# Kernel optimization log

Hardware: AMD Instinct MI355X
Metric: run time of the kernel (lower is better)

## Reference

```python
import jax, jax.numpy as jnp
import numpy as np

D = 512      # embed_dim
H = 8        # num_heads
DEPTH = 3    # decoder layers
V = 10000    # vocab_size
B = 64       # batch
NIMG = 144   # image grid tokens
SEQ = 17     # caption length (get_clip_mat(17,144))
FF = 4 * D


def layer_norm(x, g, b, eps=1e-5):
    m = jnp.mean(x, axis=-1, keepdims=True)
    v = jnp.mean((x - m) ** 2, axis=-1, keepdims=True)
    return (x - m) * jax.lax.rsqrt(v + eps) * g + b


def mha(xq, xkv, wq, bq, wk, bk, wv, bv, wo, bo):
    # torch MultiHeadSelfAttention with mask=None
    Bq, Nq, Dm = xq.shape
    hd = Dm // H
    q = (xq @ wq + bq).reshape(Bq, Nq, H, hd)
    k = (xkv @ wk + bk).reshape(Bq, -1, H, hd)
    v = (xkv @ wv + bv).reshape(Bq, -1, H, hd)
    attn = jnp.einsum('bqhd,bkhd->bhqk', q, k) * (hd ** -0.5)
    attn = jax.nn.softmax(attn, axis=-1)
    out = jnp.einsum('bhqk,bkhd->bqhd', attn, v).reshape(Bq, Nq, Dm)
    return out @ wo + bo


def setup_inputs() -> dict:
    key = jax.random.key(0)
    ks = iter(jax.random.split(key, 64))
    def p(*shape):
        return jax.random.normal(next(ks), shape, dtype=jnp.float32) * 0.02
    inp = {
        'encoder_out': jax.random.normal(next(ks), (B, NIMG, D), dtype=jnp.float32),
        'w': jax.random.uniform(next(ks), (SEQ, NIMG), dtype=jnp.float32) / NIMG,
        # img2text: Linear + LayerNorm
        'i2t_w': p(D, D), 'i2t_b': jnp.zeros((D,), jnp.float32),
        'i2t_ln_g': jnp.ones((D,), jnp.float32), 'i2t_ln_b': jnp.zeros((D,), jnp.float32),
        'emb': p(V, D),                                   # word_embed table
        'gen_w': p(D, V), 'gen_b': jnp.zeros((V,), jnp.float32),  # generator
        'a_w': p(2 * D, D), 'a_b': jnp.zeros((D,), jnp.float32),  # a_embed gate
        'fln_g': jnp.ones((D,), jnp.float32), 'fln_b': jnp.zeros((D,), jnp.float32),
        # stacked per-layer params [DEPTH, ...]
        'sa_wq': p(DEPTH, D, D), 'sa_bq': jnp.zeros((DEPTH, D), jnp.float32),
        'sa_wk': p(DEPTH, D, D), 'sa_bk': jnp.zeros((DEPTH, D), jnp.float32),
        'sa_wv': p(DEPTH, D, D), 'sa_bv': jnp.zeros((DEPTH, D), jnp.float32),
        'sa_wo': p(DEPTH, D, D), 'sa_bo': jnp.zeros((DEPTH, D), jnp.float32),
        'ca_wq': p(DEPTH, D, D), 'ca_bq': jnp.zeros((DEPTH, D), jnp.float32),
        'ca_wk': p(DEPTH, D, D), 'ca_bk': jnp.zeros((DEPTH, D), jnp.float32),
        'ca_wv': p(DEPTH, D, D), 'ca_bv': jnp.zeros((DEPTH, D), jnp.float32),
        'ca_wo': p(DEPTH, D, D), 'ca_bo': jnp.zeros((DEPTH, D), jnp.float32),
        'ln1_g': jnp.ones((DEPTH, D), jnp.float32), 'ln1_b': jnp.zeros((DEPTH, D), jnp.float32),
        'ln2_g': jnp.ones((DEPTH, D), jnp.float32), 'ln2_b': jnp.zeros((DEPTH, D), jnp.float32),
        'ln3_g': jnp.ones((DEPTH, D), jnp.float32), 'ln3_b': jnp.zeros((DEPTH, D), jnp.float32),
        'fc1_w': p(DEPTH, D, FF), 'fc1_b': jnp.zeros((DEPTH, FF), jnp.float32),
        'fc2_w': p(DEPTH, FF, D), 'fc2_b': jnp.zeros((DEPTH, D), jnp.float32),
    }
    return inp


def reference(encoder_out, w, i2t_w, i2t_b, i2t_ln_g, i2t_ln_b, emb, gen_w, gen_b,
              a_w, a_b, fln_g, fln_b,
              sa_wq, sa_bq, sa_wk, sa_bk, sa_wv, sa_bv, sa_wo, sa_bo,
              ca_wq, ca_bq, ca_wk, ca_bk, ca_wv, ca_bv, ca_wo, ca_bo,
              ln1_g, ln1_b, ln2_g, ln2_b, ln3_g, ln3_b,
              fc1_w, fc1_b, fc2_w, fc2_b):
    # img2text (dropout = eval no-op)
    text_emb = layer_norm(encoder_out @ i2t_w + i2t_b, i2t_ln_g, i2t_ln_b)  # [B,NIMG,D]
    # vocab-softmax word embedding gating
    word_prob = jax.nn.softmax(jnp.einsum('bnd,vd->bnv', text_emb, emb), axis=-1)
    word_emb = text_emb + jnp.einsum('bnv,vd->bnd', word_prob, emb)
    # map 144 image tokens -> 17 caption slots
    x = jnp.einsum('sn,bnd->bsd', w, word_emb)  # [B,SEQ,D]
    x_self = x
    for i in range(DEPTH):
        sc = x
        x = mha(x, x, sa_wq[i], sa_bq[i], sa_wk[i], sa_bk[i], sa_wv[i], sa_bv[i], sa_wo[i], sa_bo[i])
        x_self = x
        x = layer_norm(x + sc, ln1_g[i], ln1_b[i])
        sc = x
        x = mha(x, encoder_out, ca_wq[i], ca_bq[i], ca_wk[i], ca_bk[i], ca_wv[i], ca_bv[i], ca_wo[i], ca_bo[i])
        x = layer_norm(x + sc, ln2_g[i], ln2_b[i])
        sc = x
        x = jax.nn.relu(x @ fc1_w[i] + fc1_b[i]) @ fc2_w[i] + fc2_b[i]
        x = layer_norm(x + sc, ln3_g[i], ln3_b[i])
    # sigmoid-gated blend of last layer output and last self-attn output
    g = jax.nn.sigmoid(jnp.concatenate([x, x_self], axis=2) @ a_w + a_b)
    x = layer_norm(x * g + x_self * (1.0 - g), fln_g, fln_b)
    out = x @ gen_w + gen_b  # [B,SEQ,V]
    return out
```

## Files before the change

### kernel.cpp

```cpp
#include <hip/hip_runtime.h>

typedef unsigned short u16;
typedef __attribute__((ext_vector_type(8))) short s16x8;
typedef __attribute__((ext_vector_type(4))) float f32x4;

__device__ __forceinline__ u16 f2bf(float x) {
    union { float f; unsigned int u; } v; v.f = x;
    return (u16)((v.u + 0x7fffu + ((v.u >> 16) & 1u)) >> 16);
}
__device__ __forceinline__ float bf2f(u16 u) {
    union { unsigned int u; float f; } v; v.u = ((unsigned int)u) << 16;
    return v.f;
}

__device__ __forceinline__ void gload_lds16(const void* g, void* l) {
    __builtin_amdgcn_global_load_lds((const __attribute__((address_space(1))) void*)g,
                                     (__attribute__((address_space(3))) void*)l, 16, 0, 0);
}

template<int BM, int BN, int WM, int WN, int MODE>
__global__ __launch_bounds__(256)
void k_gemm(const u16* __restrict__ A, int lda, const u16* __restrict__ B, int ldb,
            float* __restrict__ Cf, int ldcf, u16* __restrict__ Cb, int ldcb,
            const float* __restrict__ bias, int relu, float* __restrict__ rowsum,
            int M, int N, int Ktot, int ksplit, long czstride)
{
    constexpr int MT = WM / 16, NT = WN / 16, WC = BN / WN;
    constexpr int AI = (BM * 4) / 256, BI = (BN * 4) / 256;
    __shared__ __align__(16) u16 As[BM * 32];
    __shared__ __align__(16) u16 Bs[BN * 32];
    int tid = threadIdx.x, w = tid >> 6, lane = tid & 63;
    int m0 = blockIdx.y * BM, n0 = blockIdx.x * BN;
    int wr = w / WC, wc = w % WC, lm = lane & 15, kq = lane >> 4;
    int kbeg = blockIdx.z * ksplit;
    int kend = kbeg + ksplit; if (kend > Ktot) kend = Ktot;
    if (czstride) Cf += (size_t)blockIdx.z * czstride;

    f32x4 acc[MT][NT] = {};

    for (int k0 = kbeg; k0 < kend; k0 += 32) {
        __syncthreads();
#pragma unroll
        for (int i = 0; i < AI; ++i) {
            int c = i * 256 + tid;
            const u16* g = A + (size_t)(m0 + (c >> 2)) * lda + k0 + ((c & 3) << 3);
            gload_lds16(g, As + (size_t)(i * 256 + w * 64) * 8);
        }
#pragma unroll
        for (int i = 0; i < BI; ++i) {
            int c = i * 256 + tid;
            const u16* g = B + (size_t)(n0 + (c >> 2)) * ldb + k0 + ((c & 3) << 3);
            gload_lds16(g, Bs + (size_t)(i * 256 + w * 64) * 8);
        }
        __syncthreads();
        s16x8 af[MT], bfr[NT];
#pragma unroll
        for (int mi = 0; mi < MT; ++mi)
            af[mi] = *(const s16x8*)&As[((wr * WM + mi * 16 + lm) << 5) + (kq << 3)];
#pragma unroll
        for (int ni = 0; ni < NT; ++ni)
            bfr[ni] = *(const s16x8*)&Bs[((wc * WN + ni * 16 + lm) << 5) + (kq << 3)];
#pragma unroll
        for (int mi = 0; mi < MT; ++mi)
#pragma unroll
            for (int ni = 0; ni < NT; ++ni)
                acc[mi][ni] = __builtin_amdgcn_mfma_f32_16x16x32_bf16(af[mi], bfr[ni], acc[mi][ni], 0, 0, 0);
    }

    if constexpr (MODE == 1) {
#pragma unroll
        for (int mi = 0; mi < MT; ++mi) {
            int rb = m0 + wr * WM + mi * 16 + kq * 4;
#pragma unroll
            for (int r = 0; r < 4; ++r) {
                int row = rb + r;
                float ps = 0.f;
#pragma unroll
                for (int ni = 0; ni < NT; ++ni) {
                    int col = n0 + wc * WN + ni * 16 + lm;
                    float e = 0.f;
                    if (col < N) { e = __expf(acc[mi][ni][r]); ps += e; }
                    if (row < M) Cb[(size_t)row * ldcb + col] = f2bf(e);
                }
                ps += __shfl_xor(ps, 1); ps += __shfl_xor(ps, 2);
                ps += __shfl_xor(ps, 4); ps += __shfl_xor(ps, 8);
                if (lm == 0 && row < M) atomicAdd(rowsum + row, ps);
            }
        }
    } else {
#pragma unroll
        for (int mi = 0; mi < MT; ++mi) {
            int rb = m0 + wr * WM + mi * 16 + kq * 4;
#pragma unroll
            for (int ni = 0; ni < NT; ++ni) {
                int col = n0 + wc * WN + ni * 16 + lm;
                if (col >= N) continue;
                float bv = bias ? bias[col] : 0.f;
#pragma unroll
                for (int r = 0; r < 4; ++r) {
                    int row = rb + r;
                    if (row >= M) continue;
                    float v = acc[mi][ni][r] + bv;
                    if (relu) v = fmaxf(v, 0.f);
                    if (Cf) Cf[(size_t)row * ldcf + col] = v;
                    if (Cb) Cb[(size_t)row * ldcb + col] = f2bf(v);
                }
            }
        }
    }
}

__global__ __launch_bounds__(256)
void k_transpose(const float* __restrict__ in, long in_zs, u16* __restrict__ out, long out_zs,
                 int R, int C, int Rpad, int Cpad, int ldout)
{
    __shared__ float tile[32][33];
    const float* src = in + (size_t)blockIdx.z * in_zs;
    u16* dst = out + (size_t)blockIdx.z * out_zs;
    int c0 = blockIdx.x * 32, r0 = blockIdx.y * 32;
    int tx = threadIdx.x, ty = threadIdx.y;
#pragma unroll
    for (int i = 0; i < 32; i += 8) {
        int r = r0 + ty + i, c = c0 + tx;
        tile[ty + i][tx] = (r < R && c < C) ? src[(size_t)r * C + c] : 0.f;
    }
    __syncthreads();
#pragma unroll
    for (int i = 0; i < 32; i += 8) {
        int c = c0 + ty + i, r = r0 + tx;
        if (c < Cpad && r < Rpad) dst[(size_t)c * ldout + r] = f2bf(tile[tx][ty + i]);
    }
}

__global__ __launch_bounds__(256)
void k_cvt(const float* __restrict__ in, u16* __restrict__ out, int n)
{
    for (int i = blockIdx.x * 256 + threadIdx.x; i < n; i += gridDim.x * 256)
        out[i] = f2bf(in[i]);
}

__global__ __launch_bounds__(256)
void k_zero(float* __restrict__ p, int n)
{
    int i = blockIdx.x * 256 + threadIdx.x;
    if (i < n) p[i] = 0.f;
}

__global__ __launch_bounds__(256)
void k_biaspack(const float* __restrict__ sbq, const float* __restrict__ sbk, const float* __restrict__ sbv,
                const float* __restrict__ cbk, const float* __restrict__ cbv,
                float* __restrict__ sout, float* __restrict__ cout)
{
    int i = blockIdx.x * 256 + threadIdx.x;
    if (i < 4608) {
        int l = i / 1536, j = i % 1536;
        sout[i] = j < 512 ? sbq[l * 512 + j] : j < 1024 ? sbk[l * 512 + j - 512] : sbv[l * 512 + j - 1024];
    }
    if (i < 3072) {
        int l = i / 1024, j = i % 1024;
        cout[i] = j < 512 ? cbk[l * 512 + j] : cbv[l * 512 + j - 512];
    }
}

__global__ __launch_bounds__(256)
void k_reduce_we(const float* __restrict__ part, long ps,
                 const float* __restrict__ text, const float* __restrict__ rs,
                 float* __restrict__ out, int n)
{
    int i = blockIdx.x * 256 + threadIdx.x;
    if (i >= n) return;
    float s = 0.f;
#pragma unroll
    for (int z = 0; z < 8; ++z) s += part[(size_t)z * ps + i];
    out[i] = text[i] + s * (1.f / rs[i >> 9]);
}

__global__ __launch_bounds__(256)
void k_ln(const float* __restrict__ xin, const float* __restrict__ res,
          const float* __restrict__ g, const float* __restrict__ b,
          float* __restrict__ out, u16* __restrict__ out_bf, int ldbf)
{
    int row = blockIdx.x, t = threadIdx.x;
    size_t base = (size_t)row * 512;
    float v0 = xin[base + t], v1 = xin[base + t + 256];
    if (res) { v0 += res[base + t]; v1 += res[base + t + 256]; }
    float s1 = v0 + v1, s2 = v0 * v0 + v1 * v1;
#pragma unroll
    for (int o = 32; o > 0; o >>= 1) { s1 += __shfl_down(s1, o); s2 += __shfl_down(s2, o); }
    __shared__ float a1[4], a2[4], mr[2];
    if ((t & 63) == 0) { a1[t >> 6] = s1; a2[t >> 6] = s2; }
    __syncthreads();
    if (t == 0) {
        float S1 = a1[0] + a1[1] + a1[2] + a1[3];
        float S2 = a2[0] + a2[1] + a2[2] + a2[3];
        float m = S1 * (1.f / 512.f);
        float var = S2 * (1.f / 512.f) - m * m;
        mr[0] = m; mr[1] = rsqrtf(var + 1e-5f);
    }
    __syncthreads();
    float m = mr[0], rs = mr[1];
    float y0 = (v0 - m) * rs * g[t] + b[t];
    float y1 = (v1 - m) * rs * g[t + 256] + b[t + 256];
    out[base + t] = y0; out[base + t + 256] = y1;
    if (out_bf) {
        size_t bb = (size_t)row * ldbf;
        out_bf[bb + t] = f2bf(y0); out_bf[bb + t + 256] = f2bf(y1);
    }
}

__global__ __launch_bounds__(256)
void k_wmap(const float* __restrict__ w, const float* __restrict__ we,
            float* __restrict__ x, u16* __restrict__ x_bf)
{
    int bid = blockIdx.x;
    int b = bid / 17, s = bid % 17;
    int t = threadIdx.x;
    const float* wr = w + s * 144;
    const float* base = we + (size_t)b * 144 * 512;
    float a0 = 0.f, a1 = 0.f;
    for (int n = 0; n < 144; ++n) {
        float wv = wr[n];
        a0 += wv * base[(size_t)n * 512 + t];
        a1 += wv * base[(size_t)n * 512 + t + 256];
    }
    size_t r = (size_t)(b * 17 + s);
    x[r * 512 + t] = a0; x[r * 512 + t + 256] = a1;
    x_bf[r * 1024 + t] = f2bf(a0); x_bf[r * 1024 + t + 256] = f2bf(a1);
}

__global__ __launch_bounds__(128)
void k_attn_self(const u16* __restrict__ qkv, u16* __restrict__ o)
{
    int b = blockIdx.x >> 3, h = blockIdx.x & 7;
    __shared__ float qs[17][65], ks[17][65], vs[17][65], ps[17][18];
    int t = threadIdx.x;
    for (int i = t; i < 17 * 64; i += 128) {
        int s = i >> 6, d = i & 63;
        size_t g = ((size_t)(b * 17 + s)) * 1536 + h * 64 + d;
        qs[s][d] = bf2f(qkv[g]); ks[s][d] = bf2f(qkv[g + 512]); vs[s][d] = bf2f(qkv[g + 1024]);
    }
    __syncthreads();
    for (int i = t; i < 17 * 17; i += 128) {
        int r = i / 17, c = i % 17;
        float a = 0.f;
#pragma unroll
        for (int d = 0; d < 64; ++d) a += qs[r][d] * ks[c][d];
        ps[r][c] = a * 0.125f;
    }
    __syncthreads();
    if (t < 17) {
        float mxv = -1e30f;
        for (int c = 0; c < 17; ++c) mxv = fmaxf(mxv, ps[t][c]);
        float sm = 0.f;
        for (int c = 0; c < 17; ++c) { float e = __expf(ps[t][c] - mxv); ps[t][c] = e; sm += e; }
        float inv = 1.f / sm;
        for (int c = 0; c < 17; ++c) ps[t][c] *= inv;
    }
    __syncthreads();
    for (int i = t; i < 17 * 64; i += 128) {
        int s = i >> 6, d = i & 63;
        float a = 0.f;
#pragma unroll
        for (int j = 0; j < 17; ++j) a += ps[s][j] * vs[j][d];
        o[((size_t)(b * 17 + s)) * 512 + h * 64 + d] = f2bf(a);
    }
}

__global__ __launch_bounds__(256)
void k_attn_cross(const u16* __restrict__ q, const u16* __restrict__ kv, u16* __restrict__ o)
{
    int b = blockIdx.x >> 3, h = blockIdx.x & 7;
    __shared__ float qs[17][65];
    __shared__ float ps[17][145];
    int t = threadIdx.x;
    for (int i = t; i < 17 * 64; i += 256) {
        int s = i >> 6, d = i & 63;
        qs[s][d] = bf2f(q[((size_t)(b * 17 + s)) * 512 + h * 64 + d]);
    }
    __syncthreads();
    for (int i = t; i < 17 * 144; i += 256) {
        int r = i / 144, c = i % 144;
        const u16* kr = kv + ((size_t)(b * 144 + c)) * 3072 + h * 64;
        float a = 0.f;
#pragma unroll
        for (int d = 0; d < 64; ++d) a += qs[r][d] * bf2f(kr[d]);
        ps[r][c] = a * 0.125f;
    }
    __syncthreads();
    if (t < 17) {
        float mxv = -1e30f;
        for (int c = 0; c < 144; ++c) mxv = fmaxf(mxv, ps[t][c]);
        float sm = 0.f;
        for (int c = 0; c < 144; ++c) { float e = __expf(ps[t][c] - mxv); ps[t][c] = e; sm += e; }
        float inv = 1.f / sm;
        for (int c = 0; c < 144; ++c) ps[t][c] *= inv;
    }
    __syncthreads();
    for (int i = t; i < 17 * 64; i += 256) {
        int s = i >> 6, d = i & 63;
        float a = 0.f;
        for (int j = 0; j < 144; ++j)
            a += ps[s][j] * bf2f(kv[((size_t)(b * 144 + j)) * 3072 + 512 + h * 64 + d]);
        o[((size_t)(b * 17 + s)) * 512 + h * 64 + d] = f2bf(a);
    }
}

__global__ __launch_bounds__(256)
void k_blend(const float* __restrict__ x, const float* __restrict__ xs,
             const float* __restrict__ gl, float* __restrict__ y, int n)
{
    int i = blockIdx.x * 256 + threadIdx.x;
    if (i < n) {
        float s = 1.f / (1.f + __expf(-gl[i]));
        y[i] = x[i] * s + xs[i] * (1.f - s);
    }
}

extern "C" void kernel_launch(void* const* d_in, const int* in_sizes, int n_in,
                              void* d_out, int out_size, void* d_ws, size_t ws_size,
                              hipStream_t stream)
{
    (void)in_sizes; (void)out_size;
    if (n_in < 39) return;
    const float* enc    = (const float*)d_in[0];
    const float* wmat   = (const float*)d_in[1];
    const float* i2t_w  = (const float*)d_in[2];
    const float* i2t_b  = (const float*)d_in[3];
    const float* i2t_g  = (const float*)d_in[4];
    const float* i2t_bb = (const float*)d_in[5];
    const float* emb    = (const float*)d_in[6];
    const float* gen_w  = (const float*)d_in[7];
    const float* gen_b  = (const float*)d_in[8];
    const float* a_w    = (const float*)d_in[9];
    const float* a_b    = (const float*)d_in[10];
    const float* fln_g  = (const float*)d_in[11];
    const float* fln_b  = (const float*)d_in[12];
    const float* sa_wq  = (const float*)d_in[13];
    const float* sa_bq  = (const float*)d_in[14];
    const float* sa_wk  = (const float*)d_in[15];
    const float* sa_bk  = (const float*)d_in[16];
    const float* sa_wv  = (const float*)d_in[17];
    const float* sa_bv  = (const float*)d_in[18];
    const float* sa_wo  = (const float*)d_in[19];
    const float* sa_bo  = (const float*)d_in[20];
    const float* ca_wq  = (const float*)d_in[21];
    const float* ca_bq  = (const float*)d_in[22];
    const float* ca_wk  = (const float*)d_in[23];
    const float* ca_bk  = (const float*)d_in[24];
    const float* ca_wv  = (const float*)d_in[25];
    const float* ca_bv  = (const float*)d_in[26];
    const float* ca_wo  = (const float*)d_in[27];
    const float* ca_bo  = (const float*)d_in[28];
    const float* ln1_g  = (const float*)d_in[29];
    const float* ln1_b  = (const float*)d_in[30];
    const float* ln2_g  = (const float*)d_in[31];
    const float* ln2_b  = (const float*)d_in[32];
    const float* ln3_g  = (const float*)d_in[33];
    const float* ln3_b  = (const float*)d_in[34];
    const float* fc1_w  = (const float*)d_in[35];
    const float* fc1_b  = (const float*)d_in[36];
    const float* fc2_w  = (const float*)d_in[37];
    const float* fc2_b  = (const float*)d_in[38];

    char* ws = (char*)d_ws;
    size_t off = 0;
    auto AL = [](size_t x) { return (x + 255) & ~(size_t)255; };
    auto alloc = [&](size_t bytes) { char* p = ws + off; off += AL(bytes); return p; };

    u16* i2t_wT  = (u16*)alloc((size_t)512 * 512 * 2);
    u16* sa_qkvT = (u16*)alloc((size_t)3 * 1536 * 512 * 2);
    u16* sa_woT  = (u16*)alloc((size_t)3 * 512 * 512 * 2);
    u16* ca_qT   = (u16*)alloc((size_t)3 * 512 * 512 * 2);
    u16* ca_kvT  = (u16*)alloc((size_t)3 * 1024 * 512 * 2);
    u16* ca_woT  = (u16*)alloc((size_t)3 * 512 * 512 * 2);
    u16* fc1T    = (u16*)alloc((size_t)3 * 2048 * 512 * 2);
    u16* fc2T    = (u16*)alloc((size_t)3 * 512 * 2048 * 2);
    u16* a_wT    = (u16*)alloc((size_t)512 * 1024 * 2);
    u16* gen_wT  = (u16*)alloc((size_t)10112 * 512 * 2);
    u16* embB    = (u16*)alloc((size_t)10112 * 512 * 2);
    u16* embT    = (u16*)alloc((size_t)512 * 10112 * 2);
    u16* enc_bf  = (u16*)alloc((size_t)9216 * 512 * 2);
    float* text_f   = (float*)alloc((size_t)9216 * 512 * 4);
    u16*   text_bf  = (u16*)alloc((size_t)9216 * 512 * 2);
    float* word_emb = (float*)alloc((size_t)9216 * 512 * 4);
    float* rowsum   = (float*)alloc(9216 * 4);
    float* sa_qkvB  = (float*)alloc(4608 * 4);
    float* ca_kvB   = (float*)alloc(3072 * 4);

    u16* enc_kv = (u16*)alloc((size_t)9216 * 3072 * 2);
    u16* xcat   = (u16*)alloc((size_t)1088 * 1024 * 2);
    u16* tqkv   = (u16*)alloc((size_t)1088 * 1536 * 2);
    u16* attnb  = (u16*)alloc((size_t)1088 * 512 * 2);
    u16* q_bf   = (u16*)alloc((size_t)1088 * 512 * 2);
    u16* ffn    = (u16*)alloc((size_t)1088 * 2048 * 2);
    float* x_f   = (float*)alloc((size_t)1088 * 512 * 4);
    float* xs_f  = (float*)alloc((size_t)1088 * 512 * 4);
    float* tmp_f = (float*)alloc((size_t)1088 * 512 * 4);
    float* glin  = (float*)alloc((size_t)1088 * 512 * 4);

    size_t lo = off;
    long budget = (ws_size > lo) ? (long)(ws_size - lo) : 0;
    long perrow = 10112L * 2 + 8L * 512 * 4;
    int chunk = (int)((budget / perrow) & ~(long)127);
    if (chunk > 9216) chunk = 9216;
    if (chunk < 128) chunk = 128;
    u16* logits = (u16*)(ws + lo);
    float* part = (float*)(ws + lo + AL((size_t)chunk * 10112 * 2));
    long pstride = (long)chunk * 512;

    dim3 tb(32, 8);
    auto T = [&](const float* in, long izs, u16* out, long ozs, int R, int C, int Rp, int Cp, int ldo, int nz) {
        k_transpose<<<dim3((Cp + 31) / 32, (Rp + 31) / 32, nz), tb, 0, stream>>>(in, izs, out, ozs, R, C, Rp, Cp, ldo);
    };
    T(i2t_w, 0, i2t_wT, 0, 512, 512, 512, 512, 512, 1);
    T(sa_wq, 512 * 512, sa_qkvT,             1536 * 512, 512, 512, 512, 512, 512, 3);
    T(sa_wk, 512 * 512, sa_qkvT + 512 * 512, 1536 * 512, 512, 512, 512, 512, 512, 3);
    T(sa_wv, 512 * 512, sa_qkvT + 1024 * 512,1536 * 512, 512, 512, 512, 512, 512, 3);
    T(sa_wo, 512 * 512, sa_woT, 512 * 512, 512, 512, 512, 512, 512, 3);
    T(ca_wq, 512 * 512, ca_qT,  512 * 512, 512, 512, 512, 512, 512, 3);
    T(ca_wk, 512 * 512, ca_kvT,             1024 * 512, 512, 512, 512, 512, 512, 3);
    T(ca_wv, 512 * 512, ca_kvT + 512 * 512, 1024 * 512, 512, 512, 512, 512, 512, 3);
    T(ca_wo, 512 * 512, ca_woT, 512 * 512, 512, 512, 512, 512, 512, 3);
    T(fc1_w, (long)512 * 2048, fc1T, (long)2048 * 512, 512, 2048, 512, 2048, 512, 3);
    T(fc2_w, (long)2048 * 512, fc2T, (long)512 * 2048, 2048, 512, 2048, 512, 2048, 3);
    T(a_w, 0, a_wT, 0, 1024, 512, 1024, 512, 1024, 1);
    T(gen_w, 0, gen_wT, 0, 512, 10000, 512, 10112, 512, 1);
    T(emb, 0, embT, 0, 10000, 512, 10112, 512, 10112, 1);
    k_cvt<<<2048, 256, 0, stream>>>(emb, embB, 10000 * 512);
    k_cvt<<<2048, 256, 0, stream>>>(enc, enc_bf, 9216 * 512);
    k_biaspack<<<18, 256, 0, stream>>>(sa_bq, sa_bk, sa_bv, ca_bk, ca_bv, sa_qkvB, ca_kvB);
    k_zero<<<36, 256, 0, stream>>>(rowsum, 9216);

    k_gemm<64, 64, 32, 32, 0><<<dim3(8, 144), 256, 0, stream>>>(
        enc_bf, 512, i2t_wT, 512, word_emb, 512, nullptr, 0, i2t_b, 0, nullptr,
        9216, 512, 512, 512, 0);
    k_ln<<<9216, 256, 0, stream>>>(word_emb, nullptr, i2t_g, i2t_bb, text_f, text_bf, 512);

    for (int r0 = 0; r0 < 9216; r0 += chunk) {
        int CR = (9216 - r0 < chunk) ? (9216 - r0) : chunk;
        k_gemm<128, 128, 64, 64, 1><<<dim3(79, CR / 128), 256, 0, stream>>>(
            text_bf + (size_t)r0 * 512, 512, embB, 512, nullptr, 0, logits, 10112,
            nullptr, 0, rowsum + r0, CR, 10000, 512, 512, 0);
        k_gemm<128, 128, 64, 64, 0><<<dim3(4, CR / 128, 8), 256, 0, stream>>>(
            logits, 10112, embT, 10112, part, 512, nullptr, 0, nullptr, 0, nullptr,
            CR, 512, 10112, 1280, pstride);
        k_reduce_we<<<(CR * 512 + 255) / 256, 256, 0, stream>>>(
            part, pstride, text_f + (size_t)r0 * 512, rowsum + r0,
            word_emb + (size_t)r0 * 512, CR * 512);
    }

    k_wmap<<<1088, 256, 0, stream>>>(wmat, word_emb, x_f, xcat);

    k_gemm<128, 128, 64, 64, 0><<<dim3(24, 72), 256, 0, stream>>>(
        enc_bf, 512, ca_kvT, 512, nullptr, 0, enc_kv, 3072, ca_kvB, 0, nullptr,
        9216, 3072, 512, 512, 0);

    for (int l = 0; l < 3; ++l) {
        size_t wo = (size_t)l * 512 * 512;
        k_gemm<64, 64, 32, 32, 0><<<dim3(24, 17), 256, 0, stream>>>(
            xcat, 1024, sa_qkvT + (size_t)l * 1536 * 512, 512, nullptr, 0, tqkv, 1536,
            sa_qkvB + l * 1536, 0, nullptr, 1088, 1536, 512, 512, 0);
        k_attn_self<<<512, 128, 0, stream>>>(tqkv, attnb);
        k_gemm<64, 64, 32, 32, 0><<<dim3(8, 17), 256, 0, stream>>>(
            attnb, 512, sa_woT + wo, 512, xs_f, 512, xcat + 512, 1024,
            sa_bo + l * 512, 0, nullptr, 1088, 512, 512, 512, 0);
        k_ln<<<1088, 256, 0, stream>>>(xs_f, x_f, ln1_g + l * 512, ln1_b + l * 512, x_f, xcat, 1024);
        k_gemm<64, 64, 32, 32, 0><<<dim3(8, 17), 256, 0, stream>>>(
            xcat, 1024, ca_qT + wo, 512, nullptr, 0, q_bf, 512,
            ca_bq + l * 512, 0, nullptr, 1088, 512, 512, 512, 0);
        k_attn_cross<<<512, 256, 0, stream>>>(q_bf, enc_kv + l * 1024, attnb);
        k_gemm<64, 64, 32, 32, 0><<<dim3(8, 17), 256, 0, stream>>>(
            attnb, 512, ca_woT + wo, 512, tmp_f, 512, nullptr, 0,
            ca_bo + l * 512, 0, nullptr, 1088, 512, 512, 512, 0);
        k_ln<<<1088, 256, 0, stream>>>(tmp_f, x_f, ln2_g + l * 512, ln2_b + l * 512, x_f, xcat, 1024);
        k_gemm<64, 64, 32, 32, 0><<<dim3(32, 17), 256, 0, stream>>>(
            xcat, 1024, fc1T + (size_t)l * 2048 * 512, 512, nullptr, 0, ffn, 2048,
            fc1_b + l * 2048, 1, nullptr, 1088, 2048, 512, 512, 0);
        k_gemm<64, 64, 32, 32, 0><<<dim3(8, 17), 256, 0, stream>>>(
            ffn, 2048, fc2T + (size_t)l * 512 * 2048, 2048, tmp_f, 512, nullptr, 0,
            fc2_b + l * 512, 0, nullptr, 1088, 512, 2048, 2048, 0);
        k_ln<<<1088, 256, 0, stream>>>(tmp_f, x_f, ln3_g + l * 512, ln3_b + l * 512, x_f, xcat, 1024);
    }

    k_gemm<64, 64, 32, 32, 0><<<dim3(8, 17), 256, 0, stream>>>(
        xcat, 1024, a_wT, 1024, glin, 512, nullptr, 0, a_b, 0, nullptr,
        1088, 512, 1024, 1024, 0);
    k_blend<<<2176, 256, 0, stream>>>(x_f, xs_f, glin, tmp_f, 1088 * 512);
    k_ln<<<1088, 256, 0, stream>>>(tmp_f, nullptr, fln_g, fln_b, x_f, xcat, 1024);

    k_gemm<64, 64, 32, 32, 0><<<dim3(157, 17), 256, 0, stream>>>(
        xcat, 1024, gen_wT, 512, (float*)d_out, 10000, nullptr, 0, gen_b, 0, nullptr,
        1088, 10000, 512, 512, 0);
}
```

Measured before the change: 1.579 ms.

## Widen GEMM K-tile with XOR-swizzled LDS, batch setup kernels, fuse blend into LN

Result: faster. 1.439 ms (-8.9%).

```diff
diff --git a/kernel.cpp b/kernel.cpp
--- a/kernel.cpp
+++ b/kernel.cpp
@@ -22,13 +22,13 @@
 __global__ __launch_bounds__(256)
 void k_gemm(const u16* __restrict__ A, int lda, const u16* __restrict__ B, int ldb,
             float* __restrict__ Cf, int ldcf, u16* __restrict__ Cb, int ldcb,
-            const float* __restrict__ bias, int relu, float* __restrict__ rowsum,
+            const float* __restrict__ bias, int relu, float* __restrict__ rspart,
             int M, int N, int Ktot, int ksplit, long czstride)
 {
     constexpr int MT = WM / 16, NT = WN / 16, WC = BN / WN;
-    constexpr int AI = (BM * 4) / 256, BI = (BN * 4) / 256;
-    __shared__ __align__(16) u16 As[BM * 32];
-    __shared__ __align__(16) u16 Bs[BN * 32];
+    constexpr int AI = BM / 32, BI = BN / 32;
+    __shared__ __align__(16) u16 As[BM * 64];
+    __shared__ __align__(16) u16 Bs[BN * 64];
     int tid = threadIdx.x, w = tid >> 6, lane = tid & 63;
     int m0 = blockIdx.y * BM, n0 = blockIdx.x * BN;
     int wr = w / WC, wc = w % WC, lm = lane & 15, kq = lane >> 4;
@@ -38,33 +38,43 @@
 
     f32x4 acc[MT][NT] = {};
 
-    for (int k0 = kbeg; k0 < kend; k0 += 32) {
+    for (int k0 = kbeg; k0 < kend; k0 += 64) {
         __syncthreads();
 #pragma unroll
         for (int i = 0; i < AI; ++i) {
-            int c = i * 256 + tid;
-            const u16* g = A + (size_t)(m0 + (c >> 2)) * lda + k0 + ((c & 3) << 3);
-            gload_lds16(g, As + (size_t)(i * 256 + w * 64) * 8);
+            int cid = i * 256 + tid;
+            int r = cid >> 3, gc = (cid & 7) ^ (r & 7);
+            gload_lds16(A + (size_t)(m0 + r) * lda + k0 + gc * 8,
+                        As + (size_t)(i * 256 + w * 64) * 8);
         }
 #pragma unroll
         for (int i = 0; i < BI; ++i) {
-            int c = i * 256 + tid;
-            const u16* g = B + (size_t)(n0 + (c >> 2)) * ldb + k0 + ((c & 3) << 3);
-            gload_lds16(g, Bs + (size_t)(i * 256 + w * 64) * 8);
+            int cid = i * 256 + tid;
+            int r = cid >> 3, gc = (cid & 7) ^ (r & 7);
+            gload_lds16(B + (size_t)(n0 + r) * ldb + k0 + gc * 8,
+                        Bs + (size_t)(i * 256 + w * 64) * 8);
         }
         __syncthreads();
-        s16x8 af[MT], bfr[NT];
-#pragma unroll
-        for (int mi = 0; mi < MT; ++mi)
-            af[mi] = *(const s16x8*)&As[((wr * WM + mi * 16 + lm) << 5) + (kq << 3)];
-#pragma unroll
-        for (int ni = 0; ni < NT; ++ni)
-            bfr[ni] = *(const s16x8*)&Bs[((wc * WN + ni * 16 + lm) << 5) + (kq << 3)];
-#pragma unroll
-        for (int mi = 0; mi < MT; ++mi)
-#pragma unroll
-            for (int ni = 0; ni < NT; ++ni)
-                acc[mi][ni] = __builtin_amdgcn_mfma_f32_16x16x32_bf16(af[mi], bfr[ni], acc[mi][ni], 0, 0, 0);
+#pragma unroll
+        for (int kk = 0; kk < 2; ++kk) {
+            int c = kk * 4 + kq;
+            s16x8 af[MT], bfr[NT];
+#pragma unroll
+            for (int mi = 0; mi < MT; ++mi) {
+                int m = wr * WM + mi * 16 + lm;
+                af[mi] = *(const s16x8*)&As[(m << 6) + ((c ^ (m & 7)) << 3)];
+            }
+#pragma unroll
+            for (int ni = 0; ni < NT; ++ni) {
+                int n = wc * WN + ni * 16 + lm;
+                bfr[ni] = *(const s16x8*)&Bs[(n << 6) + ((c ^ (n & 7)) << 3)];
+            }
+#pragma unroll
+            for (int mi = 0; mi < MT; ++mi)
+#pragma unroll
+                for (int ni = 0; ni < NT; ++ni)
+                    acc[mi][ni] = __builtin_amdgcn_mfma_f32_16x16x32_bf16(af[mi], bfr[ni], acc[mi][ni], 0, 0, 0);
+        }
     }
 
     if constexpr (MODE == 1) {
@@ -84,7 +94,7 @@
                 }
                 ps += __shfl_xor(ps, 1); ps += __shfl_xor(ps, 2);
                 ps += __shfl_xor(ps, 4); ps += __shfl_xor(ps, 8);
-                if (lm == 0 && row < M) atomicAdd(rowsum + row, ps);
+                if (lm == 0 && row < M) rspart[(size_t)blockIdx.x * M + row] = ps;
             }
         }
     } else {
@@ -111,39 +121,54 @@
 }
 
 __global__ __launch_bounds__(256)
-void k_transpose(const float* __restrict__ in, long in_zs, u16* __restrict__ out, long out_zs,
-                 int R, int C, int Rpad, int Cpad, int ldout)
+void k_finrs(const float* __restrict__ rspart, int stride, int XB,
+             float* __restrict__ rs, int n)
+{
+    int i = blockIdx.x * 256 + threadIdx.x;
+    if (i >= n) return;
+    float s = 0.f;
+    for (int x = 0; x < XB; ++x) s += rspart[(size_t)x * stride + i];
+    rs[i] = s;
+}
+
+struct TD { const float* src; u16* dst; long izs, ozs; int R, C, Rp, Cp, ldo, tx, ty, nb; };
+struct TPack { TD d[14]; int nd; };
+
+__global__ __launch_bounds__(256)
+void k_mt(TPack p)
 {
     __shared__ float tile[32][33];
-    const float* src = in + (size_t)blockIdx.z * in_zs;
-    u16* dst = out + (size_t)blockIdx.z * out_zs;
-    int c0 = blockIdx.x * 32, r0 = blockIdx.y * 32;
-    int tx = threadIdx.x, ty = threadIdx.y;
+    int id = blockIdx.x, di = 0;
+    while (di < p.nd - 1 && id >= p.d[di].nb) { id -= p.d[di].nb; ++di; }
+    TD d = p.d[di];
+    int per = d.tx * d.ty;
+    int z = id / per, rem = id - z * per;
+    int by = rem / d.tx, bx = rem - by * d.tx;
+    const float* src = d.src + (size_t)z * d.izs;
+    u16* dst = d.dst + (size_t)z * d.ozs;
+    int c0 = bx * 32, r0 = by * 32;
+    int tx = threadIdx.x & 31, ty = threadIdx.x >> 5;
 #pragma unroll
     for (int i = 0; i < 32; i += 8) {
         int r = r0 + ty + i, c = c0 + tx;
-        tile[ty + i][tx] = (r < R && c < C) ? src[(size_t)r * C + c] : 0.f;
+        tile[ty + i][tx] = (r < d.R && c < d.C) ? src[(size_t)r * d.C + c] : 0.f;
     }
     __syncthreads();
 #pragma unroll
     for (int i = 0; i < 32; i += 8) {
         int c = c0 + ty + i, r = r0 + tx;
-        if (c < Cpad && r < Rpad) dst[(size_t)c * ldout + r] = f2bf(tile[tx][ty + i]);
-    }
-}
-
-__global__ __launch_bounds__(256)
-void k_cvt(const float* __restrict__ in, u16* __restrict__ out, int n)
-{
-    for (int i = blockIdx.x * 256 + threadIdx.x; i < n; i += gridDim.x * 256)
-        out[i] = f2bf(in[i]);
-}
-
-__global__ __launch_bounds__(256)
-void k_zero(float* __restrict__ p, int n)
-{
-    int i = blockIdx.x * 256 + threadIdx.x;
-    if (i < n) p[i] = 0.f;
+        if (c < d.Cp && r < d.Rp) dst[(size_t)c * d.ldo + r] = f2bf(tile[tx][ty + i]);
+    }
+}
+
+__global__ __launch_bounds__(256)
+void k_cvt2(const float* __restrict__ in1, u16* __restrict__ out1, int n1,
+            const float* __restrict__ in2, u16* __restrict__ out2, int n2)
+{
+    for (int i = blockIdx.x * 256 + threadIdx.x; i < n1 + n2; i += gridDim.x * 256) {
+        if (i < n1) out1[i] = f2bf(in1[i]);
+        else        out2[i - n1] = f2bf(in2[i - n1]);
+    }
 }
 
 __global__ __launch_bounds__(256)
@@ -178,17 +203,24 @@
 __global__ __launch_bounds__(256)
 void k_ln(const float* __restrict__ xin, const float* __restrict__ res,
           const float* __restrict__ g, const float* __restrict__ b,
-          float* __restrict__ out, u16* __restrict__ out_bf, int ldbf)
+          float* __restrict__ out, u16* __restrict__ out_bf, int ldbf,
+          const float* __restrict__ gl, const float* __restrict__ xs)
 {
     int row = blockIdx.x, t = threadIdx.x;
     size_t base = (size_t)row * 512;
     float v0 = xin[base + t], v1 = xin[base + t + 256];
     if (res) { v0 += res[base + t]; v1 += res[base + t + 256]; }
-    float s1 = v0 + v1, s2 = v0 * v0 + v1 * v1;
-#pragma unroll
-    for (int o = 32; o > 0; o >>= 1) { s1 += __shfl_down(s1, o); s2 += __shfl_down(s2, o); }
+    if (gl) {
+        float s0 = 1.f / (1.f + __expf(-gl[base + t]));
+        float s1 = 1.f / (1.f + __expf(-gl[base + t + 256]));
+        v0 = v0 * s0 + xs[base + t] * (1.f - s0);
+        v1 = v1 * s1 + xs[base + t + 256] * (1.f - s1);
+    }
+    float s1s = v0 + v1, s2s = v0 * v0 + v1 * v1;
+#pragma unroll
+    for (int o = 32; o > 0; o >>= 1) { s1s += __shfl_down(s1s, o); s2s += __shfl_down(s2s, o); }
     __shared__ float a1[4], a2[4], mr[2];
-    if ((t & 63) == 0) { a1[t >> 6] = s1; a2[t >> 6] = s2; }
+    if ((t & 63) == 0) { a1[t >> 6] = s1s; a2[t >> 6] = s2s; }
     __syncthreads();
     if (t == 0) {
         float S1 = a1[0] + a1[1] + a1[2] + a1[3];
@@ -302,17 +334,6 @@
         for (int j = 0; j < 144; ++j)
             a += ps[s][j] * bf2f(kv[((size_t)(b * 144 + j)) * 3072 + 512 + h * 64 + d]);
         o[((size_t)(b * 17 + s)) * 512 + h * 64 + d] = f2bf(a);
-    }
-}
-
-__global__ __launch_bounds__(256)
-void k_blend(const float* __restrict__ x, const float* __restrict__ xs,
-             const float* __restrict__ gl, float* __restrict__ y, int n)
-{
-    int i = blockIdx.x * 256 + threadIdx.x;
-    if (i < n) {
-        float s = 1.f / (1.f + __expf(-gl[i]));
-        y[i] = x[i] * s + xs[i] * (1.f - s);
     }
 }
 
@@ -384,6 +405,7 @@
     u16*   text_bf  = (u16*)alloc((size_t)9216 * 512 * 2);
     float* word_emb = (float*)alloc((size_t)9216 * 512 * 4);
     float* rowsum   = (float*)alloc(9216 * 4);
+    float* rspart   = (float*)alloc((size_t)79 * 9216 * 4);
     float* sa_qkvB  = (float*)alloc(4608 * 4);
     float* ca_kvB   = (float*)alloc(3072 * 4);
 
@@ -408,39 +430,46 @@
     float* part = (float*)(ws + lo + AL((size_t)chunk * 10112 * 2));
     long pstride = (long)chunk * 512;
 
-    dim3 tb(32, 8);
-    auto T = [&](const float* in, long izs, u16* out, long ozs, int R, int C, int Rp, int Cp, int ldo, int nz) {
-        k_transpose<<<dim3((Cp + 31) / 32, (Rp + 31) / 32, nz), tb, 0, stream>>>(in, izs, out, ozs, R, C, Rp, Cp, ldo);
+    TPack tp; int nb_total = 0;
+    auto addT = [&](int idx, const float* src, long izs, u16* dst, long ozs,
+                    int R, int C, int Rp, int Cp, int ldo, int nz) {
+        TD& d = tp.d[idx];
+        d.src = src; d.dst = dst; d.izs = izs; d.ozs = ozs;
+        d.R = R; d.C = C; d.Rp = Rp; d.Cp = Cp; d.ldo = ldo;
+        d.tx = (Cp + 31) / 32; d.ty = (Rp + 31) / 32;
+        d.nb = nz * d.tx * d.ty; nb_total += d.nb;
     };
-    T(i2t_w, 0, i2t_wT, 0, 512, 512, 512, 512, 512, 1);
-    T(sa_wq, 512 * 512, sa_qkvT,             1536 * 512, 512, 512, 512, 512, 512, 3);
-    T(sa_wk, 512 * 512, sa_qkvT + 512 * 512, 1536 * 512, 512, 512, 512, 512, 512, 3);
-    T(sa_wv, 512 * 512, sa_qkvT + 1024 * 512,1536 * 512, 512, 512, 512, 512, 512, 3);
-    T(sa_wo, 512 * 512, sa_woT, 512 * 512, 512, 512, 512, 512, 512, 3);
-    T(ca_wq, 512 * 512, ca_qT,  512 * 512, 512, 512, 512, 512, 512, 3);
-    T(ca_wk, 512 * 512, ca_kvT,             1024 * 512, 512, 512, 512, 512, 512, 3);
-    T(ca_wv, 512 * 512, ca_kvT + 512 * 512, 1024 * 512, 512, 512, 512, 512, 512, 3);
-    T(ca_wo, 512 * 512, ca_woT, 512 * 512, 512, 512, 512, 512, 512, 3);
-    T(fc1_w, (long)512 * 2048, fc1T, (long)2048 * 512, 512, 2048, 512, 2048, 512, 3);
-    T(fc2_w, (long)2048 * 512, fc2T, (long)512 * 2048, 2048, 512, 2048, 512, 2048, 3);
-    T(a_w, 0, a_wT, 0, 1024, 512, 1024, 512, 1024, 1);
-    T(gen_w, 0, gen_wT, 0, 512, 10000, 512, 10112, 512, 1);
-    T(emb, 0, embT, 0, 10000, 512, 10112, 512, 10112, 1);
-    k_cvt<<<2048, 256, 0, stream>>>(emb, embB, 10000 * 512);
-    k_cvt<<<2048, 256, 0, stream>>>(enc, enc_bf, 9216 * 512);
+    addT(0,  i2t_w, 0, i2t_wT, 0, 512, 512, 512, 512, 512, 1);
+    addT(1,  sa_wq, 512 * 512, sa_qkvT,              1536 * 512, 512, 512, 512, 512, 512, 3);
+    addT(2,  sa_wk, 512 * 512, sa_qkvT + 512 * 512,  1536 * 512, 512, 512, 512, 512, 512, 3);
+    addT(3,  sa_wv, 512 * 512, sa_qkvT + 1024 * 512, 1536 * 512, 512, 512, 512, 512, 512, 3);
+    addT(4,  sa_wo, 512 * 512, sa_woT, 512 * 512, 512, 512, 512, 512, 512, 3);
+    addT(5,  ca_wq, 512 * 512, ca_qT,  512 * 512, 512, 512, 512, 512, 512, 3);
+    addT(6,  ca_wk, 512 * 512, ca_kvT,             1024 * 512, 512, 512, 512, 512, 512, 3);
+    addT(7,  ca_wv, 512 * 512, ca_kvT + 512 * 512, 1024 * 512, 512, 512, 512, 512, 512, 3);
+    addT(8,  ca_wo, 512 * 512, ca_woT, 512 * 512, 512, 512, 512, 512, 512, 3);
+    addT(9,  fc1_w, (long)512 * 2048, fc1T, (long)2048 * 512, 512, 2048, 512, 2048, 512, 3);
+    addT(10, fc2_w, (long)2048 * 512, fc2T, (long)512 * 2048, 2048, 512, 2048, 512, 2048, 3);
+    addT(11, a_w, 0, a_wT, 0, 1024, 512, 1024, 512, 1024, 1);
+    addT(12, gen_w, 0, gen_wT, 0, 512, 10000, 512, 10112, 512, 1);
+    addT(13, emb, 0, embT, 0, 10000, 512, 10112, 512, 10112, 1);
+    tp.nd = 14;
+    k_mt<<<nb_total, 256, 0, stream>>>(tp);
+    k_cvt2<<<4096, 256, 0, stream>>>(emb, embB, 10000 * 512, enc, enc_bf, 9216 * 512);
     k_biaspack<<<18, 256, 0, stream>>>(sa_bq, sa_bk, sa_bv, ca_bk, ca_bv, sa_qkvB, ca_kvB);
-    k_zero<<<36, 256, 0, stream>>>(rowsum, 9216);
-
-    k_gemm<64, 64, 32, 32, 0><<<dim3(8, 144), 256, 0, stream>>>(
+
+    k_gemm<128, 128, 64, 64, 0><<<dim3(4, 72), 256, 0, stream>>>(
         enc_bf, 512, i2t_wT, 512, word_emb, 512, nullptr, 0, i2t_b, 0, nullptr,
         9216, 512, 512, 512, 0);
-    k_ln<<<9216, 256, 0, stream>>>(word_emb, nullptr, i2t_g, i2t_bb, text_f, text_bf, 512);
+    k_ln<<<9216, 256, 0, stream>>>(word_emb, nullptr, i2t_g, i2t_bb, text_f, text_bf, 512,
+                                   nullptr, nullptr);
 
     for (int r0 = 0; r0 < 9216; r0 += chunk) {
         int CR = (9216 - r0 < chunk) ? (9216 - r0) : chunk;
         k_gemm<128, 128, 64, 64, 1><<<dim3(79, CR / 128), 256, 0, stream>>>(
             text_bf + (size_t)r0 * 512, 512, embB, 512, nullptr, 0, logits, 10112,
-            nullptr, 0, rowsum + r0, CR, 10000, 512, 512, 0);
+            nullptr, 0, rspart, CR, 10000, 512, 512, 0);
+        k_finrs<<<(CR + 255) / 256, 256, 0, stream>>>(rspart, CR, 79, rowsum + r0, CR);
         k_gemm<128, 128, 64, 64, 0><<<dim3(4, CR / 128, 8), 256, 0, stream>>>(
             logits, 10112, embT, 10112, part, 512, nullptr, 0, nullptr, 0, nullptr,
             CR, 512, 10112, 1280, pstride);
@@ -464,7 +493,8 @@
         k_gemm<64, 64, 32, 32, 0><<<dim3(8, 17), 256, 0, stream>>>(
             attnb, 512, sa_woT + wo, 512, xs_f, 512, xcat + 512, 1024,
             sa_bo + l * 512, 0, nullptr, 1088, 512, 512, 512, 0);
-        k_ln<<<1088, 256, 0, stream>>>(xs_f, x_f, ln1_g + l * 512, ln1_b + l * 512, x_f, xcat, 1024);
+        k_ln<<<1088, 256, 0, stream>>>(xs_f, x_f, ln1_g + l * 512, ln1_b + l * 512,
+                                       x_f, xcat, 1024, nullptr, nullptr);
         k_gemm<64, 64, 32, 32, 0><<<dim3(8, 17), 256, 0, stream>>>(
             xcat, 1024, ca_qT + wo, 512, nullptr, 0, q_bf, 512,
             ca_bq + l * 512, 0, nullptr, 1088, 512, 512, 512, 0);
@@ -472,23 +502,25 @@
         k_gemm<64, 64, 32, 32, 0><<<dim3(8, 17), 256, 0, stream>>>(
             attnb, 512, ca_woT + wo, 512, tmp_f, 512, nullptr, 0,
             ca_bo + l * 512, 0, nullptr, 1088, 512, 512, 512, 0);
-        k_ln<<<1088, 256, 0, stream>>>(tmp_f, x_f, ln2_g + l * 512, ln2_b + l * 512, x_f, xcat, 1024);
+        k_ln<<<1088, 256, 0, stream>>>(tmp_f, x_f, ln2_g + l * 512, ln2_b + l * 512,
+                                       x_f, xcat, 1024, nullptr, nullptr);
         k_gemm<64, 64, 32, 32, 0><<<dim3(32, 17), 256, 0, stream>>>(
             xcat, 1024, fc1T + (size_t)l * 2048 * 512, 512, nullptr, 0, ffn, 2048,
             fc1_b + l * 2048, 1, nullptr, 1088, 2048, 512, 512, 0);
         k_gemm<64, 64, 32, 32, 0><<<dim3(8, 17), 256, 0, stream>>>(
             ffn, 2048, fc2T + (size_t)l * 512 * 2048, 2048, tmp_f, 512, nullptr, 0,
             fc2_b + l * 512, 0, nullptr, 1088, 512, 2048, 2048, 0);
-        k_ln<<<1088, 256, 0, stream>>>(tmp_f, x_f, ln3_g + l * 512, ln3_b + l * 512, x_f, xcat, 1024);
+        k_ln<<<1088, 256, 0, stream>>>(tmp_f, x_f, ln3_g + l * 512, ln3_b + l * 512,
+                                       x_f, xcat, 1024, nullptr, nullptr);
     }
 
     k_gemm<64, 64, 32, 32, 0><<<dim3(8, 17), 256, 0, stream>>>(
         xcat, 1024, a_wT, 1024, glin, 512, nullptr, 0, a_b, 0, nullptr,
         1088, 512, 1024, 1024, 0);
-    k_blend<<<2176, 256, 0, stream>>>(x_f, xs_f, glin, tmp_f, 1088 * 512);
-    k_ln<<<1088, 256, 0, stream>>>(tmp_f, nullptr, fln_g, fln_b, x_f, xcat, 1024);
-
-    k_gemm<64, 64, 32, 32, 0><<<dim3(157, 17), 256, 0, stream>>>(
+    k_ln<<<1088, 256, 0, stream>>>(x_f, nullptr, fln_g, fln_b, tmp_f, xcat, 1024,
+                                   glin, xs_f);
+
+    k_gemm<64, 64, 32, 32, 0><<<dim3(158, 17), 256, 0, stream>>>(
         xcat, 1024, gen_wT, 512, (float*)d_out, 10000, nullptr, 0, gen_b, 0, nullptr,
         1088, 10000, 512, 512, 0);
 }
```
